# Kernel tuning notes

Hardware: AMD Instinct MI355X
Metric: run time of the kernel (lower is better)

The kernel has to match this reference:

```python
import jax, jax.numpy as jnp
import numpy as np

B, Q, K, DQ, DK, DV, H = 4, 256, 1024, 512, 512, 512, 128
MASK_VALUE = -1e6  # matches torch sequence_mask fill of -1000000.0


def setup_inputs() -> dict:
    key = jax.random.key(0)
    ks = jax.random.split(key, 7)
    q = jax.random.normal(ks[0], (B, Q, DQ), dtype=jnp.float32)
    k = jax.random.normal(ks[1], (B, K, DK), dtype=jnp.float32)
    v = jax.random.normal(ks[2], (B, K, DV), dtype=jnp.float32)
    valid_lens = jax.random.randint(ks[3], (B,), 1, K + 1).astype(jnp.int64)
    # Linear weights stored torch-style as [out, in]
    w_q = jax.random.normal(ks[4], (H, DQ), dtype=jnp.float32) * 0.05
    w_k = jax.random.normal(ks[5], (H, DK), dtype=jnp.float32) * 0.05
    w_v = jax.random.normal(ks[6], (H,), dtype=jnp.float32) * 0.05
    return {"q": q, "k": k, "v": v, "valid_lens": valid_lens,
            "w_q": w_q, "w_k": w_k, "w_v": w_v}


def reference(q, k, v, valid_lens, w_q, w_k, w_v):
    qh = jnp.einsum("bqd,hd->bqh", q, w_q)              # [B,Q,H]
    kh = jnp.einsum("bkd,hd->bkh", k, w_k)              # [B,K,H]
    feats = jnp.tanh(qh[:, :, None, :] + kh[:, None, :, :])  # [B,Q,K,H]
    scores = jnp.einsum("bqkh,h->bqk", feats, w_v)      # [B,Q,K]
    mask = jnp.arange(K)[None, None, :] < valid_lens[:, None, None]
    scores = jnp.where(mask, scores, MASK_VALUE)
    attn = jax.nn.softmax(scores, axis=-1)              # dropout is identity (p=0)
    return jnp.einsum("bqk,bkv->bqv", attn, v)          # [B,Q,DV]
```

## Files before the change

kernel.cpp:

```cpp
#include <hip/hip_runtime.h>

#define B_ 4
#define Q_ 256
#define K_ 1024
#define D_ 512
#define H_ 128
#define DV_ 512
#define LOG2E 1.4426950408889634f


__global__ __launch_bounds__(256) void proj_part(
    const float* __restrict__ qin, const float* __restrict__ kin,
    const float* __restrict__ wq,  const float* __restrict__ wk,
    const int* __restrict__ valid_lens, float* __restrict__ psum)
{
    __shared__ float Xs[64 * 32];
    __shared__ float Ws[64 * 128];

    const int t = threadIdx.x, bid = blockIdx.x;
    const int ds = bid & 3, tile = bid >> 2;
    const float* X; const float* W;
    int R0;
    if (tile < 32) { X = qin + (size_t)tile * 32 * D_; W = wq; R0 = tile * 32; }
    else {
        int kt = tile - 32, kb = kt >> 5, kr0 = (kt & 31) * 32;
        if (kr0 >= valid_lens[kb]) return;
        X = kin + ((size_t)kb * K_ + kr0) * D_;
        W = wk;
        R0 = 1024 + kt * 32;
    }

    const int xrow  = (t + 0) >> 4, xdq = (t & 15) * 4;
    const int xrow1 = (t + 256) >> 4;
    float4 xr0, xr1, wr8[8];

    #define LOADX(c) do { \
        xr0 = *(const float4*)&X[(size_t)xrow  * D_ + (c)*64 + xdq]; \
        xr1 = *(const float4*)&X[(size_t)xrow1 * D_ + (c)*64 + xdq]; } while (0)
    #define LOADW(c) do { \
        _Pragma("unroll") \
        for (int i = 0; i < 8; ++i) { \
            int idx = t + i * 256; \
            wr8[i] = *(const float4*)&W[(size_t)(idx >> 4) * D_ + (c)*64 + (idx & 15) * 4]; } } while (0)
    #define WRITE_LDS() do { \
        { float v[4]; *(float4*)v = xr0; \
          _Pragma("unroll") \
          for (int j = 0; j < 4; ++j) { int d = xdq + j; \
              Xs[d * 32 + (xrow ^ (((d >> 2) & 7) << 2))] = v[j]; } } \
        { float v[4]; *(float4*)v = xr1; \
          _Pragma("unroll") \
          for (int j = 0; j < 4; ++j) { int d = xdq + j; \
              Xs[d * 32 + (xrow1 ^ (((d >> 2) & 7) << 2))] = v[j]; } } \
        _Pragma("unroll") \
        for (int i = 0; i < 8; ++i) { \
            int idx = t + i * 256; int h = idx >> 4, dq = (idx & 15) * 4; \
            float v[4]; *(float4*)v = wr8[i]; \
            _Pragma("unroll") \
            for (int j = 0; j < 4; ++j) { int d = dq + j; \
                Ws[d * 128 + (h ^ (((d >> 2) & 7) << 2))] = v[j]; } } } while (0)

    const int wid = t >> 6, lane = t & 63;
    const int r0 = (lane & 7) * 4;
    const int h0 = wid * 32 + (lane >> 3) * 4;
    float c[4][4] = {};

    const int c0 = ds * 2;
    LOADX(c0); LOADW(c0);
    WRITE_LDS();

    for (int cc = 0; cc < 2; ++cc) {
        __syncthreads();
        if (cc < 1) { LOADX(c0 + 1); LOADW(c0 + 1); }
#pragma unroll 8
        for (int kk = 0; kk < 64; ++kk) {
            const int xc = ((kk >> 2) & 7) << 2;
            float xr[4], wr[4];
            *(float4*)&xr[0] = *(const float4*)&Xs[kk * 32  + (r0 ^ xc)];
            *(float4*)&wr[0] = *(const float4*)&Ws[kk * 128 + (h0 ^ xc)];
#pragma unroll
            for (int i = 0; i < 4; ++i)
#pragma unroll
                for (int j = 0; j < 4; ++j) c[i][j] = fmaf(xr[i], wr[j], c[i][j]);
        }
        __syncthreads();
        if (cc < 1) WRITE_LDS();
    }

    float* outp = psum + ((size_t)ds * 5120 + R0) * 128;
#pragma unroll
    for (int i = 0; i < 4; ++i)
        *(float4*)&outp[(size_t)(r0 + i) * 128 + h0] = *(const float4*)&c[i][0];

    #undef LOADX
    #undef LOADW
    #undef WRITE_LDS
}

__global__ __launch_bounds__(256) void proj_reduce(
    const float* __restrict__ psum, const int* __restrict__ valid_lens,
    float* __restrict__ qh_s, float4* __restrict__ kh4)
{
    int gid = blockIdx.x * 256 + threadIdx.x;
    int row = gid >> 5, c4 = gid & 31;
    int b = 0, kk = 0;
    if (row >= 1024) {
        int r = row - 1024;
        b = r >> 10; kk = r & 1023;
        if (kk >= valid_lens[b]) return;
    }
    float4 s = make_float4(0.f, 0.f, 0.f, 0.f);
#pragma unroll
    for (int ds = 0; ds < 4; ++ds) {
        float4 v = *(const float4*)&psum[((size_t)ds * 5120 + row) * 128 + c4 * 4];
        s.x += v.x; s.y += v.y; s.z += v.z; s.w += v.w;
    }
    const float SC = 2.0f * LOG2E;
    s.x *= SC; s.y *= SC; s.z *= SC; s.w *= SC;
    if (row < 1024) *(float4*)&qh_s[(size_t)row * 128 + c4 * 4] = s;
    else            kh4[((size_t)(b * 32 + c4)) * K_ + kk] = s;
}

__global__ __launch_bounds__(256) void attn_part(
    const float* __restrict__ qh_s, const float4* __restrict__ kh4,
    const float* __restrict__ wvg,  const int* __restrict__ valid_lens,
    const float* __restrict__ vin,
    float* __restrict__ s_part, float4* __restrict__ o_part)
{
    __shared__ float  qv[1024];
    __shared__ float  wvs[128];
    __shared__ float  ptmp[4][8][64];
    __shared__ float  p[8][64];
    __shared__ float  sred[8];
    __shared__ float4 otmp[8][128];

    const int t   = threadIdx.x;
    const int bid = blockIdx.x;
    const int qt  = bid & 31, kc = (bid >> 5) & 15, b = bid >> 9;
    const int q0  = qt * 8;
    const int vl  = valid_lens[b];
    const int kbase = kc * 64;
    if (kbase >= vl) return;
    const int klen = min(64, vl - kbase);

#pragma unroll
    for (int i = 0; i < 4; ++i)
        qv[t + i * 256] = qh_s[(size_t)(b*Q_ + q0) * H_ + t + i * 256];
    if (t < 128) wvs[t] = wvg[t] * (-2.0f * LOG2E);
    __syncthreads();

    const int k  = t & 63;
    const int hh = t >> 6;
    const bool active = k < klen;

    float acc[8] = {};
    if (active) {
        const float4* khp = kh4 + (size_t)b * 32 * K_ + (kbase + k)
                          + (size_t)(hh * 8) * K_;
        const int hq0 = hh * 8;
        float4 kxn = khp[0];
#pragma unroll
        for (int i = 0; i < 8; ++i) {
            float4 kx = kxn;
            int ni = (i < 7) ? i + 1 : 7;
            kxn = khp[(size_t)ni * K_];
            const int hq = hq0 + i;
            float w4[4], kxa[4];
            *(float4*)&w4[0]  = *(const float4*)&wvs[hq*4];
            *(float4*)&kxa[0] = kx;
#pragma unroll
            for (int qi = 0; qi < 8; ++qi) {
                float q4[4];
                *(float4*)&q4[0] = *(const float4*)&qv[qi*128 + hq*4];
#pragma unroll
                for (int j = 0; j < 4; ++j) {
                    float tt = __builtin_amdgcn_exp2f(q4[j] + kxa[j]);
                    float rr = __builtin_amdgcn_rcpf(tt + 1.0f);
                    acc[qi] = fmaf(w4[j], rr, acc[qi]);
                }
            }
        }
    }
#pragma unroll
    for (int qi = 0; qi < 8; ++qi) ptmp[hh][qi][k] = acc[qi];
    __syncthreads();

    {
        const int qia = hh * 2;
#pragma unroll
        for (int q2 = 0; q2 < 2; ++q2) {
            const int qi = qia + q2;
            float a = ptmp[0][qi][k] + ptmp[1][qi][k]
                    + ptmp[2][qi][k] + ptmp[3][qi][k];
            float e = active ? __builtin_amdgcn_exp2f(a) : 0.f;
            p[qi][k] = e;
            float s = e;
#pragma unroll
            for (int off = 32; off > 0; off >>= 1) s += __shfl_xor(s, off);
            if (k == 0) sred[qi] = s;
        }
    }
    __syncthreads();

    if (t < 8)
        s_part[(size_t)(b*Q_ + q0 + t) * 16 + kc] = sred[t];

    const int col  = t & 127;
    const int half = t >> 7;
    const int kb2  = half * 32;
    const int ke2  = min(klen, kb2 + 32);
    const float4* vb = (const float4*)vin + (size_t)b * K_ * 128
                     + (size_t)kbase * 128;

    float4 o[8];
#pragma unroll
    for (int qi = 0; qi < 8; ++qi) o[qi] = make_float4(0.f, 0.f, 0.f, 0.f);

    int kk = kb2;
    const int nfull = (ke2 > kb2) ? ((ke2 - kb2) >> 2) : 0;
    if (nfull > 0) {
        float4 n0v = vb[(size_t)(kk+0)*128 + col];
        float4 n1v = vb[(size_t)(kk+1)*128 + col];
        float4 n2v = vb[(size_t)(kk+2)*128 + col];
        float4 n3v = vb[(size_t)(kk+3)*128 + col];
        for (int g = 0; g < nfull; ++g) {
            float4 v0 = n0v, v1 = n1v, v2 = n2v, v3 = n3v;
            int kn = kk + 4;
            if (g + 1 < nfull) {
                n0v = vb[(size_t)(kn+0)*128 + col];
                n1v = vb[(size_t)(kn+1)*128 + col];
                n2v = vb[(size_t)(kn+2)*128 + col];
                n3v = vb[(size_t)(kn+3)*128 + col];
            }
#pragma unroll
            for (int qi = 0; qi < 8; ++qi) {
                float4 pq = *(const float4*)&p[qi][kk];
                o[qi].x += pq.x*v0.x + pq.y*v1.x + pq.z*v2.x + pq.w*v3.x;
                o[qi].y += pq.x*v0.y + pq.y*v1.y + pq.z*v2.y + pq.w*v3.y;
                o[qi].z += pq.x*v0.z + pq.y*v1.z + pq.z*v2.z + pq.w*v3.z;
                o[qi].w += pq.x*v0.w + pq.y*v1.w + pq.z*v2.w + pq.w*v3.w;
            }
            kk = kn;
        }
    }
    for (; kk < ke2; ++kk) {
        float4 v0 = vb[(size_t)kk*128 + col];
#pragma unroll
        for (int qi = 0; qi < 8; ++qi) {
            float pk = p[qi][kk];
            o[qi].x += pk*v0.x; o[qi].y += pk*v0.y;
            o[qi].z += pk*v0.z; o[qi].w += pk*v0.w;
        }
    }

    if (half == 1) {
#pragma unroll
        for (int qi = 0; qi < 8; ++qi) otmp[qi][col] = o[qi];
    }
    __syncthreads();
    if (half == 0) {
#pragma unroll
        for (int qi = 0; qi < 8; ++qi) {
            float4 r = otmp[qi][col];
            o[qi].x += r.x; o[qi].y += r.y; o[qi].z += r.z; o[qi].w += r.w;
            o_part[((size_t)kc * 1024 + (b*Q_ + q0 + qi)) * 128 + col] = o[qi];
        }
    }
}

__global__ __launch_bounds__(256) void finalize_kernel(
    const float4* __restrict__ o_part, const float* __restrict__ s_part,
    const int* __restrict__ valid_lens, float4* __restrict__ out)
{
    int gid = blockIdx.x * 256 + threadIdx.x;
    int row = gid >> 7, col = gid & 127;
    int b = row >> 8;
    int nch = (valid_lens[b] + 63) >> 6;
    float ssum = 0.f;
    float4 o = make_float4(0.f, 0.f, 0.f, 0.f);
    for (int ch = 0; ch < nch; ++ch) {
        ssum += s_part[(size_t)row * 16 + ch];
        float4 r = o_part[((size_t)ch * 1024 + row) * 128 + col];
        o.x += r.x; o.y += r.y; o.z += r.z; o.w += r.w;
    }
    float rs = __builtin_amdgcn_rcpf(ssum);
    out[gid] = make_float4(o.x*rs, o.y*rs, o.z*rs, o.w*rs);
}

extern "C" void kernel_launch(void* const* d_in, const int* in_sizes, int n_in,
                              void* d_out, int out_size, void* d_ws, size_t ws_size,
                              hipStream_t stream)
{
    const float* q  = (const float*)d_in[0];
    const float* k  = (const float*)d_in[1];
    const float* v  = (const float*)d_in[2];
    const int*   vl = (const int*)d_in[3];
    const float* wq = (const float*)d_in[4];
    const float* wk = (const float*)d_in[5];
    const float* wv = (const float*)d_in[6];
    float* out = (float*)d_out;

    float* qh_s  = (float*)d_ws;
    float* kh4   = qh_s  + (size_t)B_*Q_*H_;
    float* s_prt = kh4   + (size_t)B_*H_*K_;
    float* o_prt = s_prt + (size_t)B_*Q_*16;
    float* psum  = o_prt + (size_t)16*B_*Q_*DV_;

    proj_part      <<<dim3(640),  dim3(256), 0, stream>>>(q, k, wq, wk, vl, psum);
    proj_reduce    <<<dim3(640),  dim3(256), 0, stream>>>(psum, vl, qh_s, (float4*)kh4);
    attn_part      <<<dim3(2048), dim3(256), 0, stream>>>(qh_s, (const float4*)kh4, wv, vl, v, s_prt, (float4*)o_prt);
    finalize_kernel<<<dim3(512),  dim3(256), 0, stream>>>((const float4*)o_prt, s_prt, vl, (float4*)out);
}
```

Baseline: 115.3 us.

## Fuse split-K reductions into producer kernels via last-block atomic counters

Removes the separate proj_reduce and finalize kernels. The last block to finish a tile, detected with an atomic counter and thread fences, now does the reduction, in both the projection and the attention kernels. This cuts two kernel launches and their global round-trips. In exchange it adds a memset launch, atomics and fences, and leaves the tail reduction to a single block per group.

```diff
diff --git a/kernel.cpp b/kernel.cpp
--- a/kernel.cpp
+++ b/kernel.cpp
@@ -12,10 +12,13 @@
 __global__ __launch_bounds__(256) void proj_part(
     const float* __restrict__ qin, const float* __restrict__ kin,
     const float* __restrict__ wq,  const float* __restrict__ wk,
-    const int* __restrict__ valid_lens, float* __restrict__ psum)
+    const int* __restrict__ valid_lens, float* __restrict__ psum,
+    float* __restrict__ qh_s, float* __restrict__ khf,
+    int* __restrict__ cnt_tile)
 {
     __shared__ float Xs[64 * 32];
     __shared__ float Ws[64 * 128];
+    __shared__ int lastf;
 
     const int t = threadIdx.x, bid = blockIdx.x;
     const int ds = bid & 3, tile = bid >> 2;
@@ -91,40 +94,47 @@
     for (int i = 0; i < 4; ++i)
         *(float4*)&outp[(size_t)(r0 + i) * 128 + h0] = *(const float4*)&c[i][0];
 
+    __syncthreads();
+    if (t == 0) {
+        __threadfence();
+        int old = atomicAdd(&cnt_tile[tile], 1);
+        lastf = (old == 3);
+    }
+    __syncthreads();
+    if (!lastf) return;
+    __threadfence();
+
+    const float SC = 2.0f * LOG2E;
+#pragma unroll
+    for (int u = 0; u < 4; ++u) {
+        int unit = t + u * 256;
+        int r = unit >> 5, c4 = unit & 31;
+        float4 s = make_float4(0.f, 0.f, 0.f, 0.f);
+#pragma unroll
+        for (int d2 = 0; d2 < 4; ++d2) {
+            float4 v = *(const float4*)&psum[((size_t)d2 * 5120 + R0 + r) * 128 + c4 * 4];
+            s.x += v.x; s.y += v.y; s.z += v.z; s.w += v.w;
+        }
+        s.x *= SC; s.y *= SC; s.z *= SC; s.w *= SC;
+        if (tile < 32) {
+            *(float4*)&qh_s[(size_t)(tile * 32 + r) * 128 + c4 * 4] = s;
+        } else {
+            int kt = tile - 32, kb = kt >> 5, kr0 = (kt & 31) * 32;
+            size_t idx = ((size_t)kb * 32 + c4) * K_ + (kr0 + r);
+            *(float4*)&khf[idx * 4] = s;
+        }
+    }
     #undef LOADX
     #undef LOADW
     #undef WRITE_LDS
 }
 
-__global__ __launch_bounds__(256) void proj_reduce(
-    const float* __restrict__ psum, const int* __restrict__ valid_lens,
-    float* __restrict__ qh_s, float4* __restrict__ kh4)
-{
-    int gid = blockIdx.x * 256 + threadIdx.x;
-    int row = gid >> 5, c4 = gid & 31;
-    int b = 0, kk = 0;
-    if (row >= 1024) {
-        int r = row - 1024;
-        b = r >> 10; kk = r & 1023;
-        if (kk >= valid_lens[b]) return;
-    }
-    float4 s = make_float4(0.f, 0.f, 0.f, 0.f);
-#pragma unroll
-    for (int ds = 0; ds < 4; ++ds) {
-        float4 v = *(const float4*)&psum[((size_t)ds * 5120 + row) * 128 + c4 * 4];
-        s.x += v.x; s.y += v.y; s.z += v.z; s.w += v.w;
-    }
-    const float SC = 2.0f * LOG2E;
-    s.x *= SC; s.y *= SC; s.z *= SC; s.w *= SC;
-    if (row < 1024) *(float4*)&qh_s[(size_t)row * 128 + c4 * 4] = s;
-    else            kh4[((size_t)(b * 32 + c4)) * K_ + kk] = s;
-}
-
 __global__ __launch_bounds__(256) void attn_part(
     const float* __restrict__ qh_s, const float4* __restrict__ kh4,
     const float* __restrict__ wvg,  const int* __restrict__ valid_lens,
     const float* __restrict__ vin,
-    float* __restrict__ s_part, float4* __restrict__ o_part)
+    float* __restrict__ s_part, float4* __restrict__ o_part,
+    int* __restrict__ cnt_grp, float4* __restrict__ out)
 {
     __shared__ float  qv[1024];
     __shared__ float  wvs[128];
@@ -132,6 +142,7 @@
     __shared__ float  p[8][64];
     __shared__ float  sred[8];
     __shared__ float4 otmp[8][128];
+    __shared__ int    lastf;
 
     const int t   = threadIdx.x;
     const int bid = blockIdx.x;
@@ -141,6 +152,7 @@
     const int kbase = kc * 64;
     if (kbase >= vl) return;
     const int klen = min(64, vl - kbase);
+    const int nch  = (vl + 63) >> 6;
 
 #pragma unroll
     for (int i = 0; i < 4; ++i)
@@ -265,25 +277,32 @@
             o_part[((size_t)kc * 1024 + (b*Q_ + q0 + qi)) * 128 + col] = o[qi];
         }
     }
-}
-
-__global__ __launch_bounds__(256) void finalize_kernel(
-    const float4* __restrict__ o_part, const float* __restrict__ s_part,
-    const int* __restrict__ valid_lens, float4* __restrict__ out)
-{
-    int gid = blockIdx.x * 256 + threadIdx.x;
-    int row = gid >> 7, col = gid & 127;
-    int b = row >> 8;
-    int nch = (valid_lens[b] + 63) >> 6;
-    float ssum = 0.f;
-    float4 o = make_float4(0.f, 0.f, 0.f, 0.f);
-    for (int ch = 0; ch < nch; ++ch) {
-        ssum += s_part[(size_t)row * 16 + ch];
-        float4 r = o_part[((size_t)ch * 1024 + row) * 128 + col];
-        o.x += r.x; o.y += r.y; o.z += r.z; o.w += r.w;
-    }
-    float rs = __builtin_amdgcn_rcpf(ssum);
-    out[gid] = make_float4(o.x*rs, o.y*rs, o.z*rs, o.w*rs);
+
+    __syncthreads();
+    if (t == 0) {
+        __threadfence();
+        int old = atomicAdd(&cnt_grp[b * 32 + qt], 1);
+        lastf = (old == nch - 1);
+    }
+    __syncthreads();
+    if (!lastf) return;
+    __threadfence();
+
+#pragma unroll
+    for (int u = 0; u < 4; ++u) {
+        int unit = t + u * 256;
+        int r = unit >> 7, c = unit & 127;
+        int row = b * Q_ + q0 + r;
+        float ssum = 0.f;
+        float4 os = make_float4(0.f, 0.f, 0.f, 0.f);
+        for (int ch = 0; ch < nch; ++ch) {
+            ssum += s_part[(size_t)row * 16 + ch];
+            float4 rr = o_part[((size_t)ch * 1024 + row) * 128 + c];
+            os.x += rr.x; os.y += rr.y; os.z += rr.z; os.w += rr.w;
+        }
+        float rs = __builtin_amdgcn_rcpf(ssum);
+        out[(size_t)row * 128 + c] = make_float4(os.x*rs, os.y*rs, os.z*rs, os.w*rs);
+    }
 }
 
 extern "C" void kernel_launch(void* const* d_in, const int* in_sizes, int n_in,
@@ -304,9 +323,13 @@
     float* s_prt = kh4   + (size_t)B_*H_*K_;
     float* o_prt = s_prt + (size_t)B_*Q_*16;
     float* psum  = o_prt + (size_t)16*B_*Q_*DV_;
-
-    proj_part      <<<dim3(640),  dim3(256), 0, stream>>>(q, k, wq, wk, vl, psum);
-    proj_reduce    <<<dim3(640),  dim3(256), 0, stream>>>(psum, vl, qh_s, (float4*)kh4);
-    attn_part      <<<dim3(2048), dim3(256), 0, stream>>>(qh_s, (const float4*)kh4, wv, vl, v, s_prt, (float4*)o_prt);
-    finalize_kernel<<<dim3(512),  dim3(256), 0, stream>>>((const float4*)o_prt, s_prt, vl, (float4*)out);
+    int*   cnt   = (int*)(psum + (size_t)4*5120*128);
+
+    hipMemsetAsync(cnt, 0, 288 * sizeof(int), stream);
+
+    proj_part<<<dim3(640),  dim3(256), 0, stream>>>(
+        q, k, wq, wk, vl, psum, qh_s, kh4, cnt);
+    attn_part<<<dim3(2048), dim3(256), 0, stream>>>(
+        qh_s, (const float4*)kh4, wv, vl, v, s_prt, (float4*)o_prt,
+        cnt + 160, (float4*)out);
 }
```

Measured after the change: 174.7 us. 1.52x slower.
